# Kernel optimization log

Measured on AMD Instinct MI355X. Metric: run time of the kernel, lower is better.

Reference implementation:

```python
import jax, jax.numpy as jnp
import numpy as np

B, S, I, H = 256, 1024, 1, 512


def setup_inputs() -> dict:
    key = jax.random.key(0)
    ks = jax.random.split(key, 12)
    s = 1.0 / np.sqrt(H)
    u = lambda k, shape: jax.random.uniform(k, shape, minval=-s, maxval=s, dtype=jnp.float32)
    return {
        "inputs": jax.random.normal(ks[0], (B, S, I), dtype=jnp.float32),
        "enc_Wih": u(ks[1], (4 * H, I)),
        "enc_Whh": u(ks[2], (4 * H, H)),
        "enc_bih": u(ks[3], (4 * H,)),
        "enc_bhh": u(ks[4], (4 * H,)),
        "dec_Wih": u(ks[5], (4 * H, I)),
        "dec_Whh": u(ks[6], (4 * H, H)),
        "dec_bih": u(ks[7], (4 * H,)),
        "dec_bhh": u(ks[8], (4 * H,)),
        "lin_W": u(ks[9], (I, H)),
        "lin_b": u(ks[10], (I,)),
        "target_len": 256,
    }


def _lstm_cell(x, h, c, Wih, Whh, bih, bhh):
    # x: [B, in], h/c: [B, H]. PyTorch gate order: i, f, g, o.
    gates = x @ Wih.T + h @ Whh.T + bih + bhh  # [B, 4H]
    i, f, g, o = jnp.split(gates, 4, axis=-1)
    c_new = jax.nn.sigmoid(f) * c + jax.nn.sigmoid(i) * jnp.tanh(g)
    h_new = jax.nn.sigmoid(o) * jnp.tanh(c_new)
    return h_new, c_new


def reference(inputs, enc_Wih, enc_Whh, enc_bih, enc_bhh,
              dec_Wih, dec_Whh, dec_bih, dec_bhh, lin_W, lin_b, target_len):
    bs = inputs.shape[0]
    dt = inputs.dtype
    h0 = jnp.zeros((bs, H), dt)
    c0 = jnp.zeros((bs, H), dt)

    # Encoder: scan over time; only final (h, c) is used downstream.
    def enc_step(carry, x_t):
        h, c = carry
        h, c = _lstm_cell(x_t, h, c, enc_Wih, enc_Whh, enc_bih, enc_bhh)
        return (h, c), None

    (h, c), _ = jax.lax.scan(enc_step, (h0, c0), jnp.swapaxes(inputs, 0, 1))

    def dec_step(carry, _):
        x, h, c = carry
        h, c = _lstm_cell(x, h, c, dec_Wih, dec_Whh, dec_bih, dec_bhh)
        out = h @ lin_W.T + lin_b  # [B, I]
        return (out, h, c), out

    x0 = inputs[:, -1, :]  # [B, I]
    _, outs = jax.lax.scan(dec_step, (x0, h, c), None, length=target_len)
    return jnp.swapaxes(outs, 0, 1)  # [B, target_len, I]
```

## Files before the change

### kernel.cpp

```cpp
#include <hip/hip_runtime.h>

#define B_    256
#define S_    1024
#define H_    512
#define G4_   2048
#define T_    256
#define NBLK  256
#define NTHR  1024
#define BB    16
#define NBG   16
#define LBN   16
#define HS2   260
#define AUXC  0x11

typedef short bf8v  __attribute__((ext_vector_type(8)));
typedef float f4v   __attribute__((ext_vector_type(4)));
typedef int   i32x4 __attribute__((ext_vector_type(4)));

typedef const __attribute__((address_space(1))) void gas_void;
typedef __attribute__((address_space(3))) void       las_void;

#define PERM_HI 0x07060302u

__global__ void fuse_dec_weights(const float* __restrict__ dec_Whh,
                                 const float* __restrict__ dec_Wih,
                                 const float* __restrict__ lin_W,
                                 const float* __restrict__ dec_bih,
                                 const float* __restrict__ dec_bhh,
                                 const float* __restrict__ lin_b,
                                 float* __restrict__ W2,
                                 float* __restrict__ dbias)
{
    int idx = blockIdx.x * 256 + threadIdx.x;
    int j = idx >> 9, k = idx & 511;
    W2[idx] = fmaf(dec_Wih[j], lin_W[k], dec_Whh[idx]);
    if (idx < G4_)
        dbias[idx] = dec_bih[idx] + dec_bhh[idx] + dec_Wih[idx] * lin_b[0];
}

__device__ __forceinline__ float fsig(float x)
{
    return __builtin_amdgcn_rcpf(1.0f + __expf(-x));
}
__device__ __forceinline__ float ftanh(float x)
{
    return fmaf(-2.0f, __builtin_amdgcn_rcpf(1.0f + __expf(2.0f * x)), 1.0f);
}

__device__ __forceinline__ void bg_barrier(unsigned* arr, int ph)
{
    __syncthreads();
    if (threadIdx.x == 0) {
        unsigned prev = __hip_atomic_fetch_add(arr, 1u, __ATOMIC_RELAXED,
                                               __HIP_MEMORY_SCOPE_AGENT);
        const unsigned target = (unsigned)(ph + 1) * LBN;
        if (prev != target - 1u) {
            while (__hip_atomic_load(arr, __ATOMIC_RELAXED,
                                     __HIP_MEMORY_SCOPE_AGENT) < target)
                __builtin_amdgcn_s_sleep(1);
        }
    }
    __syncthreads();
}

__global__ void __launch_bounds__(NTHR)
seq2seq_kernel(const float* __restrict__ inputs,
               const float* __restrict__ enc_Wih,
               const float* __restrict__ enc_bih,
               const float* __restrict__ enc_bhh,
               const float* __restrict__ dec_Wih,
               const float* __restrict__ lin_W,
               const float* __restrict__ lin_b,
               const float* __restrict__ enc_Whh,
               const float* __restrict__ W2,
               const float* __restrict__ dbias,
               unsigned* __restrict__ hiA, unsigned* __restrict__ loA,
               unsigned* __restrict__ hiB, unsigned* __restrict__ loB,
               float* __restrict__ xcor,
               unsigned* __restrict__ bars,
               float* __restrict__ out)
{
    __shared__ unsigned hs_hi[BB * HS2];
    __shared__ unsigned hs_lo[BB * HS2];
    __shared__ float gbuf[3 * 4 * 2 * 272];

    const int tid  = threadIdx.x;
    const int w    = tid >> 6;
    const int lane = tid & 63;
    const int quad = lane >> 4;
    const int mn   = lane & 15;
    const int rs   = w & 3;
    const int ks   = w >> 2;
    const int bg   = blockIdx.x & (NBG - 1);
    const int lb   = blockIdx.x >> 4;
    const int bgbase = bg * BB;
    const bool leader = (ks == 3);

    unsigned* arr = bars + bg * 64;

    i32x4 Ah[2][4], Al[2][4];
    auto loadA = [&](const float* __restrict__ W) {
        #pragma unroll
        for (int p = 0; p < 2; ++p) {
            const int grow = (mn & 3) * H_ + lb * 32 + rs * 8 + 2 * (mn >> 2) + p;
            const float* rowp = W + (size_t)grow * H_ + ks * 128 + quad * 8;
            #pragma unroll
            for (int l = 0; l < 4; ++l) {
                const float* rp = rowp + l * 32;
                float4 f0 = *(const float4*)rp;
                float4 f1 = *(const float4*)(rp + 4);
                unsigned b0 = __float_as_uint(f0.x), b1 = __float_as_uint(f0.y);
                unsigned b2 = __float_as_uint(f0.z), b3 = __float_as_uint(f0.w);
                unsigned b4 = __float_as_uint(f1.x), b5 = __float_as_uint(f1.y);
                unsigned b6 = __float_as_uint(f1.z), b7 = __float_as_uint(f1.w);
                i32x4 hi, lo;
                hi.x = __builtin_amdgcn_perm(b1, b0, PERM_HI);
                hi.y = __builtin_amdgcn_perm(b3, b2, PERM_HI);
                hi.z = __builtin_amdgcn_perm(b5, b4, PERM_HI);
                hi.w = __builtin_amdgcn_perm(b7, b6, PERM_HI);
                float r0 = f0.x - __uint_as_float(b0 & 0xffff0000u);
                float r1 = f0.y - __uint_as_float(b1 & 0xffff0000u);
                float r2 = f0.z - __uint_as_float(b2 & 0xffff0000u);
                float r3 = f0.w - __uint_as_float(b3 & 0xffff0000u);
                float r4 = f1.x - __uint_as_float(b4 & 0xffff0000u);
                float r5 = f1.y - __uint_as_float(b5 & 0xffff0000u);
                float r6 = f1.z - __uint_as_float(b6 & 0xffff0000u);
                float r7 = f1.w - __uint_as_float(b7 & 0xffff0000u);
                lo.x = __builtin_amdgcn_perm(__float_as_uint(r1), __float_as_uint(r0), PERM_HI);
                lo.y = __builtin_amdgcn_perm(__float_as_uint(r3), __float_as_uint(r2), PERM_HI);
                lo.z = __builtin_amdgcn_perm(__float_as_uint(r5), __float_as_uint(r4), PERM_HI);
                lo.w = __builtin_amdgcn_perm(__float_as_uint(r7), __float_as_uint(r6), PERM_HI);
                Ah[p][l] = hi; Al[p][l] = lo;
            }
        }
    };

    auto stage = [&](const unsigned* hi_src, const unsigned* lo_src) {
        const size_t off = (size_t)(bgbase + w) * 256 + lane * 4;
        __builtin_amdgcn_global_load_lds((gas_void*)(hi_src + off),
                                         (las_void*)(hs_hi + w * HS2), 16, 0, AUXC);
        __builtin_amdgcn_global_load_lds((gas_void*)(lo_src + off),
                                         (las_void*)(hs_lo + w * HS2), 16, 0, AUXC);
    };

    auto dots = [&](f4v& acc0, f4v& acc1) {
        acc0 = f4v{0.f, 0.f, 0.f, 0.f};
        acc1 = f4v{0.f, 0.f, 0.f, 0.f};
        #pragma unroll
        for (int l = 0; l < 4; ++l) {
            const int boff = mn * HS2 + ks * 64 + l * 16 + quad * 4;
            i32x4 bhv = *(const i32x4*)(hs_hi + boff);
            i32x4 blv = *(const i32x4*)(hs_lo + boff);
            bf8v bh = __builtin_bit_cast(bf8v, bhv);
            bf8v bl = __builtin_bit_cast(bf8v, blv);
            bf8v a0h = __builtin_bit_cast(bf8v, Ah[0][l]);
            bf8v a0l = __builtin_bit_cast(bf8v, Al[0][l]);
            bf8v a1h = __builtin_bit_cast(bf8v, Ah[1][l]);
            bf8v a1l = __builtin_bit_cast(bf8v, Al[1][l]);
            acc0 = __builtin_amdgcn_mfma_f32_16x16x32_bf16(a0h, bh, acc0, 0, 0, 0);
            acc1 = __builtin_amdgcn_mfma_f32_16x16x32_bf16(a1h, bh, acc1, 0, 0, 0);
            acc0 = __builtin_amdgcn_mfma_f32_16x16x32_bf16(a0l, bh, acc0, 0, 0, 0);
            acc1 = __builtin_amdgcn_mfma_f32_16x16x32_bf16(a1l, bh, acc1, 0, 0, 0);
            acc0 = __builtin_amdgcn_mfma_f32_16x16x32_bf16(a0h, bl, acc0, 0, 0, 0);
            acc1 = __builtin_amdgcn_mfma_f32_16x16x32_bf16(a1h, bl, acc1, 0, 0, 0);
        }
    };

    auto writegb = [&](f4v a0, f4v a1) {
        float* gp = gbuf + ((ks * 4 + rs) * 2) * 272 + quad * 68 + mn * 4;
        *(f4v*)gp = a0;
        *(f4v*)(gp + 272) = a1;
    };
    auto reduceg = [&](f4v& a0, f4v& a1) {
        const int gb = (rs * 2) * 272 + quad * 68 + mn * 4;
        a0 += *(const f4v*)(gbuf + gb);
        a0 += *(const f4v*)(gbuf + gb + 2176);
        a0 += *(const f4v*)(gbuf + gb + 4352);
        a1 += *(const f4v*)(gbuf + gb + 272);
        a1 += *(const f4v*)(gbuf + gb + 272 + 2176);
        a1 += *(const f4v*)(gbuf + gb + 272 + 4352);
    };

    auto lstm = [&](f4v g, float& cc) -> float {
        float i_ = fsig(g[0]), f_ = fsig(g[1]);
        float g_ = ftanh(g[2]), o_ = fsig(g[3]);
        float cn = fmaf(f_, cc, i_ * g_);
        cc = cn;
        return o_ * ftanh(cn);
    };

    const int pidx = lb * 16 + rs * 4 + quad;
    const int hid0 = lb * 32 + rs * 8 + 2 * quad;

    auto storeh = [&](unsigned* hn, unsigned* ln, float h0, float h1) {
        unsigned b0 = __float_as_uint(h0), b1 = __float_as_uint(h1);
        unsigned hiw = __builtin_amdgcn_perm(b1, b0, PERM_HI);
        float r0 = h0 - __uint_as_float(b0 & 0xffff0000u);
        float r1 = h1 - __uint_as_float(b1 & 0xffff0000u);
        unsigned low = __builtin_amdgcn_perm(__float_as_uint(r1),
                                             __float_as_uint(r0), PERM_HI);
        size_t pa = (size_t)(bgbase + mn) * 256 + pidx;
        __hip_atomic_store(hn + pa, hiw, __ATOMIC_RELAXED, __HIP_MEMORY_SCOPE_AGENT);
        __hip_atomic_store(ln + pa, low, __ATOMIC_RELAXED, __HIP_MEMORY_SCOPE_AGENT);
    };

    auto proj = [&]() -> float {
        const unsigned* hh = hs_hi + w * HS2 + 4 * lane;
        const unsigned* hl = hs_lo + w * HS2 + 4 * lane;
        uint4 uh = *(const uint4*)hh;
        uint4 ul = *(const uint4*)hl;
        const float4* lwp = (const float4*)(lin_W + 8 * lane);
        float4 v0 = lwp[0], v1 = lwp[1];
        #define RL(h, l) (__uint_as_float((h) << 16) + __uint_as_float((l) << 16))
        #define RH(h, l) (__uint_as_float((h) & 0xffff0000u) + __uint_as_float((l) & 0xffff0000u))
        float s = RL(uh.x, ul.x) * v0.x + RH(uh.x, ul.x) * v0.y;
        s = fmaf(RL(uh.y, ul.y), v0.z, s); s = fmaf(RH(uh.y, ul.y), v0.w, s);
        s = fmaf(RL(uh.z, ul.z), v1.x, s); s = fmaf(RH(uh.z, ul.z), v1.y, s);
        s = fmaf(RL(uh.w, ul.w), v1.z, s); s = fmaf(RH(uh.w, ul.w), v1.w, s);
        #undef RL
        #undef RH
        s += __shfl_down(s, 32); s += __shfl_down(s, 16); s += __shfl_down(s, 8);
        s += __shfl_down(s, 4);  s += __shfl_down(s, 2);  s += __shfl_down(s, 1);
        return s;
    };

    const float linb = lin_b[0];

    float encW[2][4], encB[2][4];
    if (leader) {
        #pragma unroll
        for (int p = 0; p < 2; ++p)
            #pragma unroll
            for (int g4 = 0; g4 < 4; ++g4) {
                const int j = g4 * H_ + hid0 + p;
                encW[p][g4] = enc_Wih[j];
                encB[p][g4] = enc_bih[j] + enc_bhh[j];
            }
    }

    loadA(enc_Whh);

    if (leader) {
        size_t pa = (size_t)(bgbase + mn) * 256 + pidx;
        __hip_atomic_store(hiA + pa, 0u, __ATOMIC_RELAXED, __HIP_MEMORY_SCOPE_AGENT);
        __hip_atomic_store(loA + pa, 0u, __ATOMIC_RELAXED, __HIP_MEMORY_SCOPE_AGENT);
    }

    float cc0 = 0.f, cc1 = 0.f;
    unsigned *hic = hiA, *loc = loA, *hin = hiB, *lon = loB;
    int ph = 0;

    #pragma unroll 1
    for (int t = 0; t < S_; ++t) {
        bg_barrier(arr, ph++);
        stage(hic, loc);
        float xv = leader ? inputs[(size_t)(bgbase + mn) * S_ + t] : 0.f;
        __syncthreads();
        f4v acc0, acc1;
        dots(acc0, acc1);
        if (!leader) writegb(acc0, acc1);
        __syncthreads();
        if (leader) {
            reduceg(acc0, acc1);
            #pragma unroll
            for (int g4 = 0; g4 < 4; ++g4) {
                acc0[g4] += fmaf(xv, encW[0][g4], encB[0][g4]);
                acc1[g4] += fmaf(xv, encW[1][g4], encB[1][g4]);
            }
            float h0 = lstm(acc0, cc0);
            float h1 = lstm(acc1, cc1);
            storeh(hin, lon, h0, h1);
        }
        unsigned* t1 = hic; hic = hin; hin = t1;
        unsigned* t2 = loc; loc = lon; lon = t2;
    }

    bg_barrier(arr, ph++);
    if (lb == 0) {
        stage(hic, loc);
        __syncthreads();
        float s = proj();
        if (lane == 0) {
            float x0 = inputs[(size_t)(bgbase + w) * S_ + (S_ - 1)];
            __hip_atomic_store(&xcor[bgbase + w],
                               __float_as_uint(0) * 0.f + (x0 - (s + linb)),
                               __ATOMIC_RELAXED, __HIP_MEMORY_SCOPE_AGENT);
        }
    }
    loadA(W2);

    #pragma unroll 1
    for (int t = 0; t < T_; ++t) {
        bg_barrier(arr, ph++);
        stage(hic, loc);
        f4v db0, db1;
        if (leader) {
            #pragma unroll
            for (int g4 = 0; g4 < 4; ++g4) {
                float2 d = *(const float2*)(dbias + g4 * H_ + hid0);
                db0[g4] = d.x; db1[g4] = d.y;
            }
        }
        __syncthreads();
        f4v acc0, acc1;
        dots(acc0, acc1);
        if (!leader) writegb(acc0, acc1);
        __syncthreads();
        if (lb == 0 && t > 0) {
            float s = proj();
            if (lane == 0)
                out[(size_t)(bgbase + w) * T_ + (t - 1)] = s + linb;
        }
        if (leader) {
            reduceg(acc0, acc1);
            acc0 += db0;
            acc1 += db1;
            if (t == 0) {
                float xc = __hip_atomic_load(&xcor[bgbase + mn],
                                             __ATOMIC_RELAXED, __HIP_MEMORY_SCOPE_AGENT);
                #pragma unroll
                for (int g4 = 0; g4 < 4; ++g4) {
                    float2 dw = *(const float2*)(dec_Wih + g4 * H_ + hid0);
                    acc0[g4] = fmaf(xc, dw.x, acc0[g4]);
                    acc1[g4] = fmaf(xc, dw.y, acc1[g4]);
                }
            }
            float h0 = lstm(acc0, cc0);
            float h1 = lstm(acc1, cc1);
            storeh(hin, lon, h0, h1);
        }
        unsigned* t1 = hic; hic = hin; hin = t1;
        unsigned* t2 = loc; loc = lon; lon = t2;
    }

    bg_barrier(arr, ph++);
    if (lb == 0) {
        stage(hic, loc);
        __syncthreads();
        float s = proj();
        if (lane == 0)
            out[(size_t)(bgbase + w) * T_ + (T_ - 1)] = s + linb;
    }
}

extern "C" void kernel_launch(void* const* d_in, const int* in_sizes, int n_in,
                              void* d_out, int out_size, void* d_ws, size_t ws_size,
                              hipStream_t stream)
{
    (void)in_sizes; (void)n_in; (void)out_size; (void)ws_size;

    const float* inputs  = (const float*)d_in[0];
    const float* enc_Wih = (const float*)d_in[1];
    const float* enc_Whh = (const float*)d_in[2];
    const float* enc_bih = (const float*)d_in[3];
    const float* enc_bhh = (const float*)d_in[4];
    const float* dec_Wih = (const float*)d_in[5];
    const float* dec_Whh = (const float*)d_in[6];
    const float* dec_bih = (const float*)d_in[7];
    const float* dec_bhh = (const float*)d_in[8];
    const float* lin_W   = (const float*)d_in[9];
    const float* lin_b   = (const float*)d_in[10];
    float* out = (float*)d_out;

    float* W2      = (float*)d_ws;
    float* dbias   = W2 + (size_t)G4_ * H_;
    unsigned* hiA  = (unsigned*)(dbias + G4_);
    unsigned* loA  = hiA + (size_t)B_ * 256;
    unsigned* hiB  = loA + (size_t)B_ * 256;
    unsigned* loB  = hiB + (size_t)B_ * 256;
    float* xcor    = (float*)(loB + (size_t)B_ * 256);
    unsigned* bars = (unsigned*)(xcor + B_);

    hipMemsetAsync((void*)bars, 0, NBG * 64 * sizeof(unsigned), stream);

    hipLaunchKernelGGL(fuse_dec_weights, dim3((G4_ * H_) / 256), dim3(256), 0, stream,
                       dec_Whh, dec_Wih, lin_W, dec_bih, dec_bhh, lin_b, W2, dbias);

    void* args[] = {
        (void*)&inputs, (void*)&enc_Wih, (void*)&enc_bih, (void*)&enc_bhh,
        (void*)&dec_Wih, (void*)&lin_W, (void*)&lin_b,
        (void*)&enc_Whh, (void*)&W2, (void*)&dbias,
        (void*)&hiA, (void*)&loA, (void*)&hiB, (void*)&loB,
        (void*)&xcor, (void*)&bars, (void*)&out
    };
    hipLaunchCooperativeKernel((void*)seq2seq_kernel, dim3(NBLK), dim3(NTHR),
                               args, 0, stream);
}
```

Measured before the change: 3.744 ms.

## Replace block-group barrier with per-wave arrival counters and spread projection

Replaces the leader-thread fetch-add barrier with per-wave arrival counting: each leader wave drains its stores, then increments the group counter, and a single wave spins until all 64 arrivals are in. This removes the extra __syncthreads before arrival and lets arrivals overlap. The output projection is now spread across all 16 blocks of a group, one batch row each, and delayed by a step so it runs before the wait. Decoder bias and input-weight loads are hoisted out of the loop. The spin wait no longer sleeps, which raises atomic polling traffic.

```diff
diff --git a/kernel.cpp b/kernel.cpp
--- a/kernel.cpp
+++ b/kernel.cpp
@@ -22,6 +22,16 @@
 
 #define PERM_HI 0x07060302u
 
+__device__ __forceinline__ unsigned ald(const unsigned* a)
+{
+    return __hip_atomic_load(a, __ATOMIC_RELAXED, __HIP_MEMORY_SCOPE_AGENT);
+}
+__device__ __forceinline__ void aadd(unsigned* a)
+{
+    __hip_atomic_fetch_add(a, 1u, __ATOMIC_RELAXED, __HIP_MEMORY_SCOPE_AGENT);
+}
+__device__ __forceinline__ void vm0() { asm volatile("s_waitcnt vmcnt(0)" ::: "memory"); }
+
 __global__ void fuse_dec_weights(const float* __restrict__ dec_Whh,
                                  const float* __restrict__ dec_Wih,
                                  const float* __restrict__ lin_W,
@@ -45,22 +55,6 @@
 __device__ __forceinline__ float ftanh(float x)
 {
     return fmaf(-2.0f, __builtin_amdgcn_rcpf(1.0f + __expf(2.0f * x)), 1.0f);
-}
-
-__device__ __forceinline__ void bg_barrier(unsigned* arr, int ph)
-{
-    __syncthreads();
-    if (threadIdx.x == 0) {
-        unsigned prev = __hip_atomic_fetch_add(arr, 1u, __ATOMIC_RELAXED,
-                                               __HIP_MEMORY_SCOPE_AGENT);
-        const unsigned target = (unsigned)(ph + 1) * LBN;
-        if (prev != target - 1u) {
-            while (__hip_atomic_load(arr, __ATOMIC_RELAXED,
-                                     __HIP_MEMORY_SCOPE_AGENT) < target)
-                __builtin_amdgcn_s_sleep(1);
-        }
-    }
-    __syncthreads();
 }
 
 __global__ void __launch_bounds__(NTHR)
@@ -95,6 +89,8 @@
     const int lb   = blockIdx.x >> 4;
     const int bgbase = bg * BB;
     const bool leader = (ks == 3);
+    const int pidx = lb * 16 + rs * 4 + quad;
+    const int hid0 = lb * 32 + rs * 8 + 2 * quad;
 
     unsigned* arr = bars + bg * 64;
 
@@ -189,9 +185,6 @@
         return o_ * ftanh(cn);
     };
 
-    const int pidx = lb * 16 + rs * 4 + quad;
-    const int hid0 = lb * 32 + rs * 8 + 2 * quad;
-
     auto storeh = [&](unsigned* hn, unsigned* ln, float h0, float h1) {
         unsigned b0 = __float_as_uint(h0), b1 = __float_as_uint(h1);
         unsigned hiw = __builtin_amdgcn_perm(b1, b0, PERM_HI);
@@ -204,9 +197,9 @@
         __hip_atomic_store(ln + pa, low, __ATOMIC_RELAXED, __HIP_MEMORY_SCOPE_AGENT);
     };
 
-    auto proj = [&]() -> float {
-        const unsigned* hh = hs_hi + w * HS2 + 4 * lane;
-        const unsigned* hl = hs_lo + w * HS2 + 4 * lane;
+    auto projrow = [&](int b) -> float {
+        const unsigned* hh = hs_hi + b * HS2 + 4 * lane;
+        const unsigned* hl = hs_lo + b * HS2 + 4 * lane;
         uint4 uh = *(const uint4*)hh;
         uint4 ul = *(const uint4*)hl;
         const float4* lwp = (const float4*)(lin_W + 8 * lane);
@@ -224,6 +217,11 @@
         return s;
     };
 
+    auto wait_ph = [&](int phv) {
+        const unsigned tgt = 64u * (unsigned)(phv + 1);
+        while (ald(arr) < tgt) { }
+    };
+
     const float linb = lin_b[0];
 
     float encW[2][4], encB[2][4];
@@ -244,6 +242,8 @@
         size_t pa = (size_t)(bgbase + mn) * 256 + pidx;
         __hip_atomic_store(hiA + pa, 0u, __ATOMIC_RELAXED, __HIP_MEMORY_SCOPE_AGENT);
         __hip_atomic_store(loA + pa, 0u, __ATOMIC_RELAXED, __HIP_MEMORY_SCOPE_AGENT);
+        vm0();
+        if (lane == 0) aadd(arr);
     }
 
     float cc0 = 0.f, cc1 = 0.f;
@@ -252,9 +252,11 @@
 
     #pragma unroll 1
     for (int t = 0; t < S_; ++t) {
-        bg_barrier(arr, ph++);
+        float xv = leader ? inputs[(size_t)(bgbase + mn) * S_ + t] : 0.f;
+        if (w == 15) wait_ph(ph);
+        ++ph;
+        __syncthreads();
         stage(hic, loc);
-        float xv = leader ? inputs[(size_t)(bgbase + mn) * S_ + t] : 0.f;
         __syncthreads();
         f4v acc0, acc1;
         dots(acc0, acc1);
@@ -270,47 +272,57 @@
             float h0 = lstm(acc0, cc0);
             float h1 = lstm(acc1, cc1);
             storeh(hin, lon, h0, h1);
+            vm0();
+            if (lane == 0) aadd(arr);
         }
         unsigned* t1 = hic; hic = hin; hin = t1;
         unsigned* t2 = loc; loc = lon; lon = t2;
     }
 
-    bg_barrier(arr, ph++);
-    if (lb == 0) {
-        stage(hic, loc);
-        __syncthreads();
-        float s = proj();
+    f4v db0{0.f,0.f,0.f,0.f}, db1{0.f,0.f,0.f,0.f};
+    float dwa[4] = {0,0,0,0}, dwb[4] = {0,0,0,0};
+    if (w == 15) wait_ph(ph);
+    ++ph;
+    __syncthreads();
+    stage(hic, loc);
+    __syncthreads();
+    if (w == 0) {
+        float s = projrow(lb);
         if (lane == 0) {
-            float x0 = inputs[(size_t)(bgbase + w) * S_ + (S_ - 1)];
-            __hip_atomic_store(&xcor[bgbase + w],
-                               __float_as_uint(0) * 0.f + (x0 - (s + linb)),
+            float x0 = inputs[(size_t)(bgbase + lb) * S_ + (S_ - 1)];
+            __hip_atomic_store(&xcor[bgbase + lb], x0 - (s + linb),
                                __ATOMIC_RELAXED, __HIP_MEMORY_SCOPE_AGENT);
         }
     }
     loadA(W2);
+    if (leader) {
+        #pragma unroll
+        for (int g4 = 0; g4 < 4; ++g4) {
+            float2 d = *(const float2*)(dbias + g4 * H_ + hid0);
+            db0[g4] = d.x; db1[g4] = d.y;
+            float2 dw = *(const float2*)(dec_Wih + g4 * H_ + hid0);
+            dwa[g4] = dw.x; dwb[g4] = dw.y;
+        }
+    }
+    __syncthreads();
+    if (leader && lane == 0) aadd(arr);
 
     #pragma unroll 1
     for (int t = 0; t < T_; ++t) {
-        bg_barrier(arr, ph++);
+        if (w == 0 && t >= 2) {
+            float s = projrow(lb);
+            if (lane == 0)
+                out[(size_t)(bgbase + lb) * T_ + (t - 2)] = s + linb;
+        }
+        if (w == 15) wait_ph(ph);
+        ++ph;
+        __syncthreads();
         stage(hic, loc);
-        f4v db0, db1;
-        if (leader) {
-            #pragma unroll
-            for (int g4 = 0; g4 < 4; ++g4) {
-                float2 d = *(const float2*)(dbias + g4 * H_ + hid0);
-                db0[g4] = d.x; db1[g4] = d.y;
-            }
-        }
         __syncthreads();
         f4v acc0, acc1;
         dots(acc0, acc1);
         if (!leader) writegb(acc0, acc1);
         __syncthreads();
-        if (lb == 0 && t > 0) {
-            float s = proj();
-            if (lane == 0)
-                out[(size_t)(bgbase + w) * T_ + (t - 1)] = s + linb;
-        }
         if (leader) {
             reduceg(acc0, acc1);
             acc0 += db0;
@@ -320,26 +332,34 @@
                                              __ATOMIC_RELAXED, __HIP_MEMORY_SCOPE_AGENT);
                 #pragma unroll
                 for (int g4 = 0; g4 < 4; ++g4) {
-                    float2 dw = *(const float2*)(dec_Wih + g4 * H_ + hid0);
-                    acc0[g4] = fmaf(xc, dw.x, acc0[g4]);
-                    acc1[g4] = fmaf(xc, dw.y, acc1[g4]);
+                    acc0[g4] = fmaf(xc, dwa[g4], acc0[g4]);
+                    acc1[g4] = fmaf(xc, dwb[g4], acc1[g4]);
                 }
             }
             float h0 = lstm(acc0, cc0);
             float h1 = lstm(acc1, cc1);
             storeh(hin, lon, h0, h1);
+            vm0();
+            if (lane == 0) aadd(arr);
         }
         unsigned* t1 = hic; hic = hin; hin = t1;
         unsigned* t2 = loc; loc = lon; lon = t2;
     }
 
-    bg_barrier(arr, ph++);
-    if (lb == 0) {
-        stage(hic, loc);
-        __syncthreads();
-        float s = proj();
+    if (w == 15) wait_ph(ph);
+    __syncthreads();
+    if (w == 0) {
+        float s = projrow(lb);
         if (lane == 0)
-            out[(size_t)(bgbase + w) * T_ + (T_ - 1)] = s + linb;
+            out[(size_t)(bgbase + lb) * T_ + (T_ - 2)] = s + linb;
+    }
+    __syncthreads();
+    stage(hic, loc);
+    __syncthreads();
+    if (w == 0) {
+        float s = projrow(lb);
+        if (lane == 0)
+            out[(size_t)(bgbase + lb) * T_ + (T_ - 1)] = s + linb;
     }
 }
 
@@ -366,9 +386,9 @@
     float* dbias   = W2 + (size_t)G4_ * H_;
     unsigned* hiA  = (unsigned*)(dbias + G4_);
     unsigned* loA  = hiA + (size_t)B_ * 256;
-    unsigned* hiB  = loA + (size_t)B_ * 256;
-    unsigned* loB  = hiB + (size_t)B_ * 256;
-    float* xcor    = (float*)(loB + (size_t)B_ * 256);
+    unsigned* loB  = hiA + (size_t)B_ * 256 * 3;
+    unsigned* hiB  = hiA + (size_t)B_ * 256 * 2;
+    float* xcor    = (float*)(hiA + (size_t)B_ * 256 * 4);
     unsigned* bars = (unsigned*)(xcor + B_);
 
     hipMemsetAsync((void*)bars, 0, NBG * 64 * sizeof(unsigned), stream);
```

Measured after the change: 5.976 ms. +59.6%, slower.

## Replace atomic-counter group barrier with per-wave publish flags polled by one wave

Applied to the files above, without the earlier changes.

Replaces the per-batch-group atomic fetch_add barrier with per-producer flags: each leader wave waits for its h stores to complete, then writes a phase number to its own flag slot, and wave 0 of every block polls all 64 flags with one vector load and __all. This removes the extra __syncthreads and the serialized atomic RMW before each step, shortening the critical path of the recurrent loop. It also moves the W2 load ahead of the projection so it overlaps the encoder-to-decoder handoff. It relies on relaxed stores plus a vmcnt wait for ordering, and adds a bounded spin that silently exits after a timeout.

```diff
diff --git a/kernel.cpp b/kernel.cpp
--- a/kernel.cpp
+++ b/kernel.cpp
@@ -22,6 +22,16 @@
 
 #define PERM_HI 0x07060302u
 
+__device__ __forceinline__ unsigned ald(const unsigned* a)
+{
+    return __hip_atomic_load(a, __ATOMIC_RELAXED, __HIP_MEMORY_SCOPE_AGENT);
+}
+__device__ __forceinline__ void ast(unsigned* a, unsigned v)
+{
+    __hip_atomic_store(a, v, __ATOMIC_RELAXED, __HIP_MEMORY_SCOPE_AGENT);
+}
+__device__ __forceinline__ void vm0() { asm volatile("s_waitcnt vmcnt(0)" ::: "memory"); }
+
 __global__ void fuse_dec_weights(const float* __restrict__ dec_Whh,
                                  const float* __restrict__ dec_Wih,
                                  const float* __restrict__ lin_W,
@@ -45,22 +55,6 @@
 __device__ __forceinline__ float ftanh(float x)
 {
     return fmaf(-2.0f, __builtin_amdgcn_rcpf(1.0f + __expf(2.0f * x)), 1.0f);
-}
-
-__device__ __forceinline__ void bg_barrier(unsigned* arr, int ph)
-{
-    __syncthreads();
-    if (threadIdx.x == 0) {
-        unsigned prev = __hip_atomic_fetch_add(arr, 1u, __ATOMIC_RELAXED,
-                                               __HIP_MEMORY_SCOPE_AGENT);
-        const unsigned target = (unsigned)(ph + 1) * LBN;
-        if (prev != target - 1u) {
-            while (__hip_atomic_load(arr, __ATOMIC_RELAXED,
-                                     __HIP_MEMORY_SCOPE_AGENT) < target)
-                __builtin_amdgcn_s_sleep(1);
-        }
-    }
-    __syncthreads();
 }
 
 __global__ void __launch_bounds__(NTHR)
@@ -95,15 +89,18 @@
     const int lb   = blockIdx.x >> 4;
     const int bgbase = bg * BB;
     const bool leader = (ks == 3);
-
-    unsigned* arr = bars + bg * 64;
+    const int pidx = lb * 16 + rs * 4 + quad;
+    const int hid0 = lb * 32 + rs * 8 + 2 * quad;
+
+    unsigned* fl     = bars + bg * 64;
+    unsigned* myflag = fl + lb * 4 + rs;
 
     i32x4 Ah[2][4], Al[2][4];
-    auto loadA = [&](const float* __restrict__ W) {
+    auto loadA = [&](const float* __restrict__ Wm) {
         #pragma unroll
         for (int p = 0; p < 2; ++p) {
             const int grow = (mn & 3) * H_ + lb * 32 + rs * 8 + 2 * (mn >> 2) + p;
-            const float* rowp = W + (size_t)grow * H_ + ks * 128 + quad * 8;
+            const float* rowp = Wm + (size_t)grow * H_ + ks * 128 + quad * 8;
             #pragma unroll
             for (int l = 0; l < 4; ++l) {
                 const float* rp = rowp + l * 32;
@@ -189,9 +186,6 @@
         return o_ * ftanh(cn);
     };
 
-    const int pidx = lb * 16 + rs * 4 + quad;
-    const int hid0 = lb * 32 + rs * 8 + 2 * quad;
-
     auto storeh = [&](unsigned* hn, unsigned* ln, float h0, float h1) {
         unsigned b0 = __float_as_uint(h0), b1 = __float_as_uint(h1);
         unsigned hiw = __builtin_amdgcn_perm(b1, b0, PERM_HI);
@@ -200,8 +194,8 @@
         unsigned low = __builtin_amdgcn_perm(__float_as_uint(r1),
                                              __float_as_uint(r0), PERM_HI);
         size_t pa = (size_t)(bgbase + mn) * 256 + pidx;
-        __hip_atomic_store(hn + pa, hiw, __ATOMIC_RELAXED, __HIP_MEMORY_SCOPE_AGENT);
-        __hip_atomic_store(ln + pa, low, __ATOMIC_RELAXED, __HIP_MEMORY_SCOPE_AGENT);
+        ast(hn + pa, hiw);
+        ast(ln + pa, low);
     };
 
     auto proj = [&]() -> float {
@@ -224,6 +218,17 @@
         return s;
     };
 
+    unsigned wd = 0;
+    auto wait_ph = [&](unsigned tgt) {
+        const unsigned* fp = fl + lane;
+        for (;;) {
+            unsigned v = ald(fp);
+            if (__all((int)(v >= tgt))) break;
+            if (++wd > (1u << 26)) break;
+            __builtin_amdgcn_s_sleep(1);
+        }
+    };
+
     const float linb = lin_b[0];
 
     float encW[2][4], encB[2][4];
@@ -242,17 +247,20 @@
 
     if (leader) {
         size_t pa = (size_t)(bgbase + mn) * 256 + pidx;
-        __hip_atomic_store(hiA + pa, 0u, __ATOMIC_RELAXED, __HIP_MEMORY_SCOPE_AGENT);
-        __hip_atomic_store(loA + pa, 0u, __ATOMIC_RELAXED, __HIP_MEMORY_SCOPE_AGENT);
+        ast(hiA + pa, 0u);
+        ast(loA + pa, 0u);
+        vm0();
+        if (lane == 0) ast(myflag, 1u);
     }
 
     float cc0 = 0.f, cc1 = 0.f;
     unsigned *hic = hiA, *loc = loA, *hin = hiB, *lon = loB;
-    int ph = 0;
+    unsigned ph = 1;
 
     #pragma unroll 1
     for (int t = 0; t < S_; ++t) {
-        bg_barrier(arr, ph++);
+        if (w == 0) wait_ph(ph);
+        __syncthreads();
         stage(hic, loc);
         float xv = leader ? inputs[(size_t)(bgbase + mn) * S_ + t] : 0.f;
         __syncthreads();
@@ -270,28 +278,37 @@
             float h0 = lstm(acc0, cc0);
             float h1 = lstm(acc1, cc1);
             storeh(hin, lon, h0, h1);
-        }
+            vm0();
+            if (lane == 0) ast(myflag, ph + 1);
+        }
+        ++ph;
         unsigned* t1 = hic; hic = hin; hin = t1;
         unsigned* t2 = loc; loc = lon; lon = t2;
     }
 
-    bg_barrier(arr, ph++);
+    if (w == 0) wait_ph(ph);
+    __syncthreads();
+    if (lb == 0) stage(hic, loc);
+    loadA(W2);
     if (lb == 0) {
-        stage(hic, loc);
         __syncthreads();
         float s = proj();
         if (lane == 0) {
             float x0 = inputs[(size_t)(bgbase + w) * S_ + (S_ - 1)];
-            __hip_atomic_store(&xcor[bgbase + w],
-                               __float_as_uint(0) * 0.f + (x0 - (s + linb)),
-                               __ATOMIC_RELAXED, __HIP_MEMORY_SCOPE_AGENT);
-        }
-    }
-    loadA(W2);
+            ast((unsigned*)&xcor[bgbase + w], __float_as_uint(x0 - (s + linb)));
+        }
+    }
+    __syncthreads();
+    if (leader) {
+        vm0();
+        if (lane == 0) ast(myflag, ph + 1);
+    }
+    ++ph;
 
     #pragma unroll 1
     for (int t = 0; t < T_; ++t) {
-        bg_barrier(arr, ph++);
+        if (w == 0) wait_ph(ph);
+        __syncthreads();
         stage(hic, loc);
         f4v db0, db1;
         if (leader) {
@@ -316,8 +333,8 @@
             acc0 += db0;
             acc1 += db1;
             if (t == 0) {
-                float xc = __hip_atomic_load(&xcor[bgbase + mn],
-                                             __ATOMIC_RELAXED, __HIP_MEMORY_SCOPE_AGENT);
+                float xc = __uint_as_float(
+                    ald((const unsigned*)&xcor[bgbase + mn]));
                 #pragma unroll
                 for (int g4 = 0; g4 < 4; ++g4) {
                     float2 dw = *(const float2*)(dec_Wih + g4 * H_ + hid0);
@@ -328,12 +345,16 @@
             float h0 = lstm(acc0, cc0);
             float h1 = lstm(acc1, cc1);
             storeh(hin, lon, h0, h1);
-        }
+            vm0();
+            if (lane == 0) ast(myflag, ph + 1);
+        }
+        ++ph;
         unsigned* t1 = hic; hic = hin; hin = t1;
         unsigned* t2 = loc; loc = lon; lon = t2;
     }
 
-    bg_barrier(arr, ph++);
+    if (w == 0) wait_ph(ph);
+    __syncthreads();
     if (lb == 0) {
         stage(hic, loc);
         __syncthreads();
```

Measured after the change: 9.928 ms. 2.65x slower.
